# Performance work log

Measured on AMD Instinct MI355X. Metric: run time of the kernel, lower is better.

Reference implementation:

```python
import jax, jax.numpy as jnp
import numpy as np

N_NODES = 50000
N_EDGES = 1600000
IN_FEATS = 256
ENC_H = 20
DEC_H = 64
BIAS = 0.0  # forward arg default
TEMPERATURE = 1.0


def setup_inputs() -> dict:
    key = jax.random.key(0)
    ks = jax.random.split(key, 8)
    x = jax.random.normal(ks[0], (N_NODES, IN_FEATS), dtype=jnp.float32)
    edge_index = jax.random.randint(ks[1], (2, N_EDGES), 0, N_NODES, dtype=jnp.int64)
    node_id = 42
    # GCNConv params (glorot-ish scale)
    W_gcn = jax.random.normal(ks[2], (IN_FEATS, ENC_H), dtype=jnp.float32) / np.sqrt(IN_FEATS)
    b_gcn = jnp.zeros((ENC_H,), dtype=jnp.float32)
    # decoder MLP params
    W1 = jax.random.normal(ks[3], (3 * ENC_H, DEC_H), dtype=jnp.float32) / np.sqrt(3 * ENC_H)
    b1 = jnp.zeros((DEC_H,), dtype=jnp.float32)
    W2 = jax.random.normal(ks[4], (DEC_H, 1), dtype=jnp.float32) / np.sqrt(DEC_H)
    b2 = jnp.zeros((1,), dtype=jnp.float32)
    return {"x": x, "edge_index": edge_index, "node_id": node_id,
            "W_gcn": W_gcn, "b_gcn": b_gcn, "W1": W1, "b1": b1, "W2": W2, "b2": b2}


def _gcn_conv(x, edge_index, W, b):
    """PyG GCNConv: add self loops, symmetric normalization, sum aggregation."""
    n = x.shape[0]
    xw = x @ W  # [N, ENC_H]
    loop = jnp.arange(n, dtype=edge_index.dtype)
    row = jnp.concatenate([edge_index[0], loop])  # source
    col = jnp.concatenate([edge_index[1], loop])  # target
    ones = jnp.ones(row.shape[0], dtype=x.dtype)
    deg = jax.ops.segment_sum(ones, col, num_segments=n)
    dinv = jnp.where(deg > 0, jax.lax.rsqrt(jnp.maximum(deg, 1e-12)), 0.0)
    norm = dinv[row] * dinv[col]  # [E+N]
    msgs = xw[row] * norm[:, None]
    out = jax.ops.segment_sum(msgs, col, num_segments=n)
    return out + b


def reference(x, edge_index, node_id, W_gcn, b_gcn, W1, b1, W2, b2):
    # encoder: GCN + ReLU
    enc = jax.nn.relu(_gcn_conv(x, edge_index, W_gcn, b_gcn))  # [N, ENC_H]
    # edge representation: [row_embed | col_embed | node_embed]
    rows, cols = edge_index[0], edge_index[1]
    node_embed = jnp.broadcast_to(enc[node_id], (rows.shape[0], enc.shape[1]))
    z = jnp.concatenate([enc[rows], enc[cols], node_embed], axis=1)  # [E, 3*ENC_H]
    # decoder MLP
    h = jax.nn.relu(z @ W1 + b1)
    out_dec = h @ W2 + b2  # [E, 1]
    # Gumbel-sigmoid sampling (training=True path)
    bias = BIAS + 0.0001
    u = jax.random.uniform(jax.random.key(123), out_dec.shape, dtype=out_dec.dtype)
    eps = (bias - (1.0 - bias)) * u + (1.0 - bias)  # in (bias, 1-bias)
    gate = jnp.log(eps) - jnp.log1p(-eps)
    return jax.nn.sigmoid((gate + out_dec) / TEMPERATURE)
```

## Files before the change

### kernel.cpp

```cpp
#include <hip/hip_runtime.h>
#include <hip/hip_bf16.h>

#define IN_FEATS 256
#define ENC_H    20
#define DEC_H    64
#define EPB      8192

__device__ __forceinline__ unsigned int rotl32(unsigned int x, int d) {
  return (x << d) | (x >> (32 - d));
}

__device__ __forceinline__ void threefry2x32(unsigned int k0, unsigned int k1,
                                             unsigned int x0, unsigned int x1,
                                             unsigned int& o0, unsigned int& o1) {
  unsigned int ks0 = k0, ks1 = k1, ks2 = k0 ^ k1 ^ 0x1BD11BDAu;
  x0 += ks0; x1 += ks1;
  x0 += x1; x1 = rotl32(x1, 13); x1 ^= x0;
  x0 += x1; x1 = rotl32(x1, 15); x1 ^= x0;
  x0 += x1; x1 = rotl32(x1, 26); x1 ^= x0;
  x0 += x1; x1 = rotl32(x1,  6); x1 ^= x0;
  x0 += ks1; x1 += ks2 + 1u;
  x0 += x1; x1 = rotl32(x1, 17); x1 ^= x0;
  x0 += x1; x1 = rotl32(x1, 29); x1 ^= x0;
  x0 += x1; x1 = rotl32(x1, 16); x1 ^= x0;
  x0 += x1; x1 = rotl32(x1, 24); x1 ^= x0;
  x0 += ks2; x1 += ks0 + 2u;
  x0 += x1; x1 = rotl32(x1, 13); x1 ^= x0;
  x0 += x1; x1 = rotl32(x1, 15); x1 ^= x0;
  x0 += x1; x1 = rotl32(x1, 26); x1 ^= x0;
  x0 += x1; x1 = rotl32(x1,  6); x1 ^= x0;
  x0 += ks0; x1 += ks1 + 3u;
  x0 += x1; x1 = rotl32(x1, 17); x1 ^= x0;
  x0 += x1; x1 = rotl32(x1, 29); x1 ^= x0;
  x0 += x1; x1 = rotl32(x1, 16); x1 ^= x0;
  x0 += x1; x1 = rotl32(x1, 24); x1 ^= x0;
  x0 += ks1; x1 += ks2 + 4u;
  x0 += x1; x1 = rotl32(x1, 13); x1 ^= x0;
  x0 += x1; x1 = rotl32(x1, 15); x1 ^= x0;
  x0 += x1; x1 = rotl32(x1, 26); x1 ^= x0;
  x0 += x1; x1 = rotl32(x1,  6); x1 ^= x0;
  x0 += ks2; x1 += ks0 + 5u;
  o0 = x0; o1 = x1;
}

__device__ __forceinline__ float2 bf2_unpack(unsigned int u) {
  float2 f;
  f.x = __uint_as_float(u << 16);
  f.y = __uint_as_float(u & 0xffff0000u);
  return f;
}


__global__ __launch_bounds__(1024) void k_binhist(const int* __restrict__ row,
                                                  const int* __restrict__ col,
                                                  int* __restrict__ bbc,
                                                  unsigned int* __restrict__ rc,
                                                  int E, int nbins) {
  __shared__ int h[256];
  int t = threadIdx.x;
  if (t < 256) h[t] = 0;
  __syncthreads();
  int lo = blockIdx.x * EPB;
  int hi = min(lo + EPB, E);
  for (int e = lo + t; e < hi; e += 1024) {
    int c = col[e];
    atomicAdd(&h[c >> 8], 1);
    rc[e] = (unsigned int)row[e] | ((unsigned int)c << 16);
  }
  __syncthreads();
  if (t < nbins) bbc[blockIdx.x * nbins + t] = h[t];
}

__global__ void k_colA(const int* __restrict__ bbc, int* __restrict__ base,
                       int* __restrict__ binTot, int nblk, int nbins) {
  __shared__ int sd[256];
  int t = threadIdx.x;
  int bin = blockIdx.x;
  int v = (t < nblk) ? bbc[(size_t)t * nbins + bin] : 0;
  sd[t] = v;
  __syncthreads();
#pragma unroll
  for (int off = 1; off < 256; off <<= 1) {
    int tmp = (t >= off) ? sd[t - off] : 0;
    __syncthreads();
    sd[t] += tmp;
    __syncthreads();
  }
  if (t < nblk) base[(size_t)t * nbins + bin] = sd[t] - v;
  if (t == 255) binTot[bin] = sd[255];
}

__global__ void k_colB(const int* __restrict__ binTot, int* __restrict__ binStart, int nbins) {
  __shared__ int sd[256];
  int t = threadIdx.x;
  int v = (t < nbins) ? binTot[t] : 0;
  sd[t] = v;
  __syncthreads();
#pragma unroll
  for (int off = 1; off < 256; off <<= 1) {
    int tmp = (t >= off) ? sd[t - off] : 0;
    __syncthreads();
    sd[t] += tmp;
    __syncthreads();
  }
  if (t < nbins) {
    binStart[t] = sd[t] - v;
    if (t == nbins - 1) binStart[nbins] = sd[t];
  }
}

__global__ __launch_bounds__(1024) void k_binscatter(const unsigned int* __restrict__ rc,
                                                     const int* __restrict__ base,
                                                     const int* __restrict__ binStart,
                                                     unsigned int* __restrict__ binned,
                                                     int E, int nbins) {
  __shared__ int cur[256];
  int t = threadIdx.x;
  if (t < nbins) cur[t] = binStart[t] + base[(size_t)blockIdx.x * nbins + t];
  __syncthreads();
  int lo = blockIdx.x * EPB;
  int hi = min(lo + EPB, E);
  for (int e = lo + t; e < hi; e += 1024) {
    unsigned int v = rc[e];
    int slot = atomicAdd(&cur[v >> 24], 1);
    binned[slot] = v;
  }
}

__global__ __launch_bounds__(1024) void k_binsort(const unsigned int* __restrict__ binned,
                                                  const int* __restrict__ binStart,
                                                  unsigned short* __restrict__ sorted_r,
                                                  int* __restrict__ nstart,
                                                  float* __restrict__ dinv,
                                                  int N, int E) {
  __shared__ int cnt[256];
  __shared__ int ls[256];
  __shared__ int cur[256];
  int t = threadIdx.x;
  int bin = blockIdx.x;
  if (t < 256) cnt[t] = 0;
  __syncthreads();
  int s = binStart[bin], epos = binStart[bin + 1];
  for (int i = s + t; i < epos; i += 1024)
    atomicAdd(&cnt[(binned[i] >> 16) & 0xFFu], 1);
  __syncthreads();
  int v = (t < 256) ? cnt[t] : 0;
  if (t < 256) ls[t] = v;
  __syncthreads();
#pragma unroll
  for (int off = 1; off < 256; off <<= 1) {
    int tmp = 0;
    if (t < 256 && t >= off) tmp = ls[t - off];
    __syncthreads();
    if (t < 256 && t >= off) ls[t] += tmp;
    __syncthreads();
  }
  if (t < 256) {
    int ex = ls[t] - v;
    cur[t] = s + ex;
    int n = (bin << 8) + t;
    if (n < N) {
      nstart[n] = s + ex;
      dinv[n] = rsqrtf((float)(v + 1));
    }
  }
  if (bin == 0 && t == 0) nstart[N] = E;
  __syncthreads();
  for (int i = s + t; i < epos; i += 1024) {
    unsigned int e32 = binned[i];
    int cl = (int)((e32 >> 16) & 0xFFu);
    int slot = atomicAdd(&cur[cl], 1);
    sorted_r[slot] = (unsigned short)(e32 & 0xFFFFu);
  }
}


__global__ void k_xw(const float* __restrict__ x, const float* __restrict__ W,
                     const float* __restrict__ dinv, __hip_bfloat16* __restrict__ xwd, int N) {
  __shared__ float Wl[IN_FEATS * ENC_H];
  for (int i = threadIdx.x; i < IN_FEATS * ENC_H; i += blockDim.x) Wl[i] = W[i];
  __syncthreads();
  int g = blockIdx.x * blockDim.x + threadIdx.x;
  int n = g >> 2, part = g & 3;
  if (n >= N) return;
  float acc[ENC_H];
#pragma unroll
  for (int j = 0; j < ENC_H; j++) acc[j] = 0.0f;
  const float4* x4 = reinterpret_cast<const float4*>(x + (size_t)n * IN_FEATS);
#pragma unroll 4
  for (int k4 = 0; k4 < 16; k4++) {
    float4 v = x4[k4 * 4 + part];
    int kbase = k4 * 16 + part * 4;
    const float* w0 = &Wl[(kbase + 0) * ENC_H];
    const float* w1 = &Wl[(kbase + 1) * ENC_H];
    const float* w2 = &Wl[(kbase + 2) * ENC_H];
    const float* w3 = &Wl[(kbase + 3) * ENC_H];
#pragma unroll
    for (int j = 0; j < ENC_H; j++) {
      acc[j] = fmaf(v.x, w0[j], acc[j]);
      acc[j] = fmaf(v.y, w1[j], acc[j]);
      acc[j] = fmaf(v.z, w2[j], acc[j]);
      acc[j] = fmaf(v.w, w3[j], acc[j]);
    }
  }
#pragma unroll
  for (int j = 0; j < ENC_H; j++) acc[j] += __shfl_xor(acc[j], 1);
#pragma unroll
  for (int j = 0; j < ENC_H; j++) acc[j] += __shfl_xor(acc[j], 2);
  float d = dinv[n];
  __hip_bfloat16* o = xwd + (size_t)n * ENC_H;
  int jb = part * 5;
#pragma unroll
  for (int jj = 0; jj < 5; jj++) o[jb + jj] = __float2bfloat16(acc[jb + jj] * d);
}

__global__ void k_gather(const int* __restrict__ nstart,
                         const unsigned short* __restrict__ sorted_r,
                         const __hip_bfloat16* __restrict__ xwd, const float* __restrict__ dinv,
                         const float* __restrict__ bg, float* __restrict__ enc, int N) {
  int t = blockIdx.x * blockDim.x + threadIdx.x;
  int n = t / ENC_H;
  int j = t % ENC_H;
  if (n >= N) return;
  int s = nstart[n], epos = nstart[n + 1];
  float acc = __bfloat162float(xwd[(size_t)n * ENC_H + j]);
  for (int k = s; k < epos; k++) {
    int r = (int)sorted_r[k];
    acc += __bfloat162float(xwd[(size_t)r * ENC_H + j]);
  }
  float v = acc * dinv[n] + bg[j];
  enc[(size_t)n * ENC_H + j] = fmaxf(v, 0.0f);
}

__global__ void k_pq(const float* __restrict__ enc, const float* __restrict__ W1,
                     __hip_bfloat16* __restrict__ Pq, __hip_bfloat16* __restrict__ Qq, int N) {
  __shared__ float Wl[2 * ENC_H * DEC_H];
  for (int i = threadIdx.x; i < 2 * ENC_H * DEC_H; i += blockDim.x) Wl[i] = W1[i];
  __syncthreads();
  int t = blockIdx.x * blockDim.x + threadIdx.x;
  int n = t / DEC_H, j = t % DEC_H;
  if (n >= N) return;
  const float* en = enc + (size_t)n * ENC_H;
  float p = 0.0f, q = 0.0f;
#pragma unroll
  for (int k = 0; k < ENC_H; k++) {
    float ev = en[k];
    p = fmaf(ev, Wl[k * DEC_H + j], p);
    q = fmaf(ev, Wl[(k + ENC_H) * DEC_H + j], q);
  }
  size_t idx = (size_t)(j >> 4) * N * 16 + (size_t)n * 16 + (j & 15);
  Pq[idx] = __float2bfloat16(p);
  Qq[idx] = __float2bfloat16(q);
}

__global__ void k_t3(const float* __restrict__ enc, const float* __restrict__ W1,
                     const float* __restrict__ b1, const int* __restrict__ node_id,
                     float* __restrict__ t3) {
  int j = threadIdx.x;
  int nid = node_id[0];
  const float* en = enc + (size_t)nid * ENC_H;
  float a = b1[j];
#pragma unroll
  for (int k = 0; k < ENC_H; k++) a = fmaf(en[k], W1[(2 * ENC_H + k) * DEC_H + j], a);
  t3[j] = a;
}

template <int Q4>
__global__ void k_dec_q(const unsigned int* __restrict__ rc,
                        const __hip_bfloat16* __restrict__ Pq,
                        const __hip_bfloat16* __restrict__ Qq,
                        const float* __restrict__ t3, const float* __restrict__ W2,
                        const float* __restrict__ b2,
                        float* __restrict__ partial, float* __restrict__ out,
                        int N, int E) {
  __shared__ float t3l[16], w2l[16];
  if (threadIdx.x < 16) {
    t3l[threadIdx.x] = t3[Q4 * 16 + threadIdx.x];
    w2l[threadIdx.x] = W2[Q4 * 16 + threadIdx.x];
  }
  __syncthreads();
  int e = blockIdx.x * blockDim.x + threadIdx.x;
  if (e >= E) return;
  unsigned int v = rc[e];
  int r = (int)(v & 0xFFFFu);
  int c = (int)(v >> 16);
  const __hip_bfloat16* Pbase = Pq + (size_t)Q4 * N * 16;
  const __hip_bfloat16* Qbase = Qq + (size_t)Q4 * N * 16;
  const uint4* pr = reinterpret_cast<const uint4*>(Pbase + (size_t)r * 16);
  const uint4* qc = reinterpret_cast<const uint4*>(Qbase + (size_t)c * 16);
  float acc = 0.0f;
#pragma unroll
  for (int b = 0; b < 2; b++) {
    uint4 pu = pr[b];
    uint4 qu = qc[b];
    int j0 = b * 8;
    float2 p0 = bf2_unpack(pu.x), q0 = bf2_unpack(qu.x);
    float2 p1 = bf2_unpack(pu.y), q1 = bf2_unpack(qu.y);
    float2 p2 = bf2_unpack(pu.z), q2 = bf2_unpack(qu.z);
    float2 p3 = bf2_unpack(pu.w), q3 = bf2_unpack(qu.w);
    float h;
    h = fmaxf(p0.x + q0.x + t3l[j0 + 0], 0.0f); acc = fmaf(h, w2l[j0 + 0], acc);
    h = fmaxf(p0.y + q0.y + t3l[j0 + 1], 0.0f); acc = fmaf(h, w2l[j0 + 1], acc);
    h = fmaxf(p1.x + q1.x + t3l[j0 + 2], 0.0f); acc = fmaf(h, w2l[j0 + 2], acc);
    h = fmaxf(p1.y + q1.y + t3l[j0 + 3], 0.0f); acc = fmaf(h, w2l[j0 + 3], acc);
    h = fmaxf(p2.x + q2.x + t3l[j0 + 4], 0.0f); acc = fmaf(h, w2l[j0 + 4], acc);
    h = fmaxf(p2.y + q2.y + t3l[j0 + 5], 0.0f); acc = fmaf(h, w2l[j0 + 5], acc);
    h = fmaxf(p3.x + q3.x + t3l[j0 + 6], 0.0f); acc = fmaf(h, w2l[j0 + 6], acc);
    h = fmaxf(p3.y + q3.y + t3l[j0 + 7], 0.0f); acc = fmaf(h, w2l[j0 + 7], acc);
  }
  if (Q4 == 0) {
    partial[e] = acc;
  } else if (Q4 < 3) {
    partial[e] += acc;
  } else {
    float od = partial[e] + acc + b2[0];
    unsigned int o0, o1;
    threefry2x32(0u, 123u, 0u, (unsigned int)e, o0, o1);
    unsigned int bits = o0 ^ o1;
    float u = __uint_as_float((bits >> 9) | 0x3f800000u) - 1.0f;
    float eps = (-0.9998f) * u + 0.9999f;
    float gate = logf(eps) - log1pf(-eps);
    float s = 1.0f / (1.0f + expf(-(gate + od)));
    out[e] = s;
  }
}

extern "C" void kernel_launch(void* const* d_in, const int* in_sizes, int n_in,
                              void* d_out, int out_size, void* d_ws, size_t ws_size,
                              hipStream_t stream) {
  const float* x       = (const float*)d_in[0];
  const int*   edge    = (const int*)d_in[1];
  const int*   node_id = (const int*)d_in[2];
  const float* W_gcn   = (const float*)d_in[3];
  const float* b_gcn   = (const float*)d_in[4];
  const float* W1      = (const float*)d_in[5];
  const float* b1      = (const float*)d_in[6];
  const float* W2      = (const float*)d_in[7];
  const float* b2      = (const float*)d_in[8];
  float* out = (float*)d_out;

  int N = in_sizes[0] / IN_FEATS;
  int E = in_sizes[1] / 2;
  const int* erow = edge;
  const int* ecol = edge + E;
  int nbins = (N + 255) >> 8;
  int NB = (E + EPB - 1) / EPB;

  char* ws = (char*)d_ws;
  size_t off = 0;
  auto alloc = [&](size_t bytes) {
    char* p = ws + off;
    off = (off + bytes + 255) & ~(size_t)255;
    return p;
  };
  __hip_bfloat16* xwd = (__hip_bfloat16*)alloc((size_t)N * ENC_H * sizeof(__hip_bfloat16));
  float* enc  = (float*)alloc((size_t)N * ENC_H * sizeof(float));
  float* dinv = (float*)alloc((size_t)N * sizeof(float));
  int*  nstart = (int*)alloc((size_t)(N + 1) * sizeof(int));
  unsigned int*   rc       = (unsigned int*)alloc((size_t)E * sizeof(unsigned int));
  unsigned int*   binned   = (unsigned int*)alloc((size_t)E * sizeof(unsigned int));
  unsigned short* sorted_r = (unsigned short*)alloc((size_t)E * sizeof(unsigned short));
  int* bbc      = (int*)alloc((size_t)NB * nbins * sizeof(int));
  int* base     = (int*)alloc((size_t)NB * nbins * sizeof(int));
  int* binTot   = (int*)alloc((size_t)nbins * sizeof(int));
  int* binStart = (int*)alloc((size_t)(nbins + 1) * sizeof(int));
  __hip_bfloat16* Pq = (__hip_bfloat16*)alloc((size_t)N * DEC_H * sizeof(__hip_bfloat16));
  __hip_bfloat16* Qq = (__hip_bfloat16*)alloc((size_t)N * DEC_H * sizeof(__hip_bfloat16));
  float* partial = (float*)alloc((size_t)E * sizeof(float));
  float* t3   = (float*)alloc((size_t)DEC_H * sizeof(float));
  (void)ws_size; (void)n_in; (void)out_size;

  const int B = 256;
  int ge  = (E + B - 1) / B;
  int gxw = (N * 4 + B - 1) / B;
  int gg  = (N * ENC_H + B - 1) / B;
  int gpq = (N * DEC_H + B - 1) / B;

  k_binhist   <<<NB, 1024, 0, stream>>>(erow, ecol, bbc, rc, E, nbins);
  k_colA      <<<nbins, 256, 0, stream>>>(bbc, base, binTot, NB, nbins);
  k_colB      <<<1, 256, 0, stream>>>(binTot, binStart, nbins);
  k_binscatter<<<NB, 1024, 0, stream>>>(rc, base, binStart, binned, E, nbins);
  k_binsort   <<<nbins, 1024, 0, stream>>>(binned, binStart, sorted_r, nstart, dinv, N, E);
  k_xw        <<<gxw, B, 0, stream>>>(x, W_gcn, dinv, xwd, N);
  k_gather    <<<gg, B, 0, stream>>>(nstart, sorted_r, xwd, dinv, b_gcn, enc, N);
  k_pq        <<<gpq, B, 0, stream>>>(enc, W1, Pq, Qq, N);
  k_t3        <<<1, DEC_H, 0, stream>>>(enc, W1, b1, node_id, t3);
  k_dec_q<0>  <<<ge, B, 0, stream>>>(rc, Pq, Qq, t3, W2, b2, partial, out, N, E);
  k_dec_q<1>  <<<ge, B, 0, stream>>>(rc, Pq, Qq, t3, W2, b2, partial, out, N, E);
  k_dec_q<2>  <<<ge, B, 0, stream>>>(rc, Pq, Qq, t3, W2, b2, partial, out, N, E);
  k_dec_q<3>  <<<ge, B, 0, stream>>>(rc, Pq, Qq, t3, W2, b2, partial, out, N, E);
}
```

Measured before the change: 197.2 us.

## Fuse four quarter-decoder passes into one kernel with multiple edges per thread

The four templated decoder launches, each covering 16 of the 64 hidden units and passing a per-edge partial sum through global memory, become one kernel. Each thread handles four edges and keeps their accumulators in registers across the quarters. This removes the partial buffer's global reads and writes and three launches. The original split was likely there to keep each quarter's Pq/Qq slice cache-resident; the fused loop adds a __syncthreads after each quarter so the block walks the slices together, but cache locality across the whole grid may still be worse.

Result: slower. 240.7 us (+22.0%).

```diff
diff --git a/kernel.cpp b/kernel.cpp
--- a/kernel.cpp
+++ b/kernel.cpp
@@ -5,6 +5,7 @@
 #define ENC_H    20
 #define DEC_H    64
 #define EPB      8192
+#define EPT      4
 
 __device__ __forceinline__ unsigned int rotl32(unsigned int x, int d) {
   return (x << d) | (x >> (32 - d));
@@ -265,55 +266,71 @@
   t3[j] = a;
 }
 
-template <int Q4>
-__global__ void k_dec_q(const unsigned int* __restrict__ rc,
-                        const __hip_bfloat16* __restrict__ Pq,
-                        const __hip_bfloat16* __restrict__ Qq,
-                        const float* __restrict__ t3, const float* __restrict__ W2,
-                        const float* __restrict__ b2,
-                        float* __restrict__ partial, float* __restrict__ out,
-                        int N, int E) {
-  __shared__ float t3l[16], w2l[16];
-  if (threadIdx.x < 16) {
-    t3l[threadIdx.x] = t3[Q4 * 16 + threadIdx.x];
-    w2l[threadIdx.x] = W2[Q4 * 16 + threadIdx.x];
-  }
-  __syncthreads();
-  int e = blockIdx.x * blockDim.x + threadIdx.x;
-  if (e >= E) return;
-  unsigned int v = rc[e];
-  int r = (int)(v & 0xFFFFu);
-  int c = (int)(v >> 16);
-  const __hip_bfloat16* Pbase = Pq + (size_t)Q4 * N * 16;
-  const __hip_bfloat16* Qbase = Qq + (size_t)Q4 * N * 16;
-  const uint4* pr = reinterpret_cast<const uint4*>(Pbase + (size_t)r * 16);
-  const uint4* qc = reinterpret_cast<const uint4*>(Qbase + (size_t)c * 16);
-  float acc = 0.0f;
-#pragma unroll
-  for (int b = 0; b < 2; b++) {
-    uint4 pu = pr[b];
-    uint4 qu = qc[b];
-    int j0 = b * 8;
-    float2 p0 = bf2_unpack(pu.x), q0 = bf2_unpack(qu.x);
-    float2 p1 = bf2_unpack(pu.y), q1 = bf2_unpack(qu.y);
-    float2 p2 = bf2_unpack(pu.z), q2 = bf2_unpack(qu.z);
-    float2 p3 = bf2_unpack(pu.w), q3 = bf2_unpack(qu.w);
-    float h;
-    h = fmaxf(p0.x + q0.x + t3l[j0 + 0], 0.0f); acc = fmaf(h, w2l[j0 + 0], acc);
-    h = fmaxf(p0.y + q0.y + t3l[j0 + 1], 0.0f); acc = fmaf(h, w2l[j0 + 1], acc);
-    h = fmaxf(p1.x + q1.x + t3l[j0 + 2], 0.0f); acc = fmaf(h, w2l[j0 + 2], acc);
-    h = fmaxf(p1.y + q1.y + t3l[j0 + 3], 0.0f); acc = fmaf(h, w2l[j0 + 3], acc);
-    h = fmaxf(p2.x + q2.x + t3l[j0 + 4], 0.0f); acc = fmaf(h, w2l[j0 + 4], acc);
-    h = fmaxf(p2.y + q2.y + t3l[j0 + 5], 0.0f); acc = fmaf(h, w2l[j0 + 5], acc);
-    h = fmaxf(p3.x + q3.x + t3l[j0 + 6], 0.0f); acc = fmaf(h, w2l[j0 + 6], acc);
-    h = fmaxf(p3.y + q3.y + t3l[j0 + 7], 0.0f); acc = fmaf(h, w2l[j0 + 7], acc);
-  }
-  if (Q4 == 0) {
-    partial[e] = acc;
-  } else if (Q4 < 3) {
-    partial[e] += acc;
-  } else {
-    float od = partial[e] + acc + b2[0];
+__global__ void k_dec(const unsigned int* __restrict__ rc,
+                      const __hip_bfloat16* __restrict__ Pq,
+                      const __hip_bfloat16* __restrict__ Qq,
+                      const float* __restrict__ t3, const float* __restrict__ W2,
+                      const float* __restrict__ b2,
+                      float* __restrict__ out, int N, int E) {
+  __shared__ float t3l[DEC_H], w2l[DEC_H];
+  if (threadIdx.x < DEC_H) {
+    t3l[threadIdx.x] = t3[threadIdx.x];
+    w2l[threadIdx.x] = W2[threadIdx.x];
+  }
+  __syncthreads();
+  int base = blockIdx.x * (blockDim.x * EPT) + threadIdx.x;
+  unsigned int rcv[EPT];
+  float acc[EPT];
+#pragma unroll
+  for (int i = 0; i < EPT; i++) {
+    int e = base + i * 256;
+    rcv[i] = (e < E) ? rc[e] : 0u;
+    acc[i] = 0.0f;
+  }
+#pragma unroll
+  for (int q = 0; q < 4; q++) {
+    const __hip_bfloat16* Pb = Pq + (size_t)q * N * 16;
+    const __hip_bfloat16* Qb = Qq + (size_t)q * N * 16;
+#pragma unroll
+    for (int i = 0; i < EPT; i++) {
+      int e = base + i * 256;
+      if (e < E) {
+        unsigned int v = rcv[i];
+        int r = (int)(v & 0xFFFFu);
+        int c = (int)(v >> 16);
+        const uint4* pr = reinterpret_cast<const uint4*>(Pb + (size_t)r * 16);
+        const uint4* qc = reinterpret_cast<const uint4*>(Qb + (size_t)c * 16);
+        float a = acc[i];
+#pragma unroll
+        for (int b = 0; b < 2; b++) {
+          uint4 pu = pr[b];
+          uint4 qu = qc[b];
+          int j0 = q * 16 + b * 8;
+          float2 p0 = bf2_unpack(pu.x), q0 = bf2_unpack(qu.x);
+          float2 p1 = bf2_unpack(pu.y), q1 = bf2_unpack(qu.y);
+          float2 p2 = bf2_unpack(pu.z), q2 = bf2_unpack(qu.z);
+          float2 p3 = bf2_unpack(pu.w), q3 = bf2_unpack(qu.w);
+          float h;
+          h = fmaxf(p0.x + q0.x + t3l[j0 + 0], 0.0f); a = fmaf(h, w2l[j0 + 0], a);
+          h = fmaxf(p0.y + q0.y + t3l[j0 + 1], 0.0f); a = fmaf(h, w2l[j0 + 1], a);
+          h = fmaxf(p1.x + q1.x + t3l[j0 + 2], 0.0f); a = fmaf(h, w2l[j0 + 2], a);
+          h = fmaxf(p1.y + q1.y + t3l[j0 + 3], 0.0f); a = fmaf(h, w2l[j0 + 3], a);
+          h = fmaxf(p2.x + q2.x + t3l[j0 + 4], 0.0f); a = fmaf(h, w2l[j0 + 4], a);
+          h = fmaxf(p2.y + q2.y + t3l[j0 + 5], 0.0f); a = fmaf(h, w2l[j0 + 5], a);
+          h = fmaxf(p3.x + q3.x + t3l[j0 + 6], 0.0f); a = fmaf(h, w2l[j0 + 6], a);
+          h = fmaxf(p3.y + q3.y + t3l[j0 + 7], 0.0f); a = fmaf(h, w2l[j0 + 7], a);
+        }
+        acc[i] = a;
+      }
+    }
+    __syncthreads();
+  }
+  float bias2 = b2[0];
+#pragma unroll
+  for (int i = 0; i < EPT; i++) {
+    int e = base + i * 256;
+    if (e >= E) continue;
+    float od = acc[i] + bias2;
     unsigned int o0, o1;
     threefry2x32(0u, 123u, 0u, (unsigned int)e, o0, o1);
     unsigned int bits = o0 ^ o1;
@@ -366,15 +383,14 @@
   int* binStart = (int*)alloc((size_t)(nbins + 1) * sizeof(int));
   __hip_bfloat16* Pq = (__hip_bfloat16*)alloc((size_t)N * DEC_H * sizeof(__hip_bfloat16));
   __hip_bfloat16* Qq = (__hip_bfloat16*)alloc((size_t)N * DEC_H * sizeof(__hip_bfloat16));
-  float* partial = (float*)alloc((size_t)E * sizeof(float));
   float* t3   = (float*)alloc((size_t)DEC_H * sizeof(float));
   (void)ws_size; (void)n_in; (void)out_size;
 
   const int B = 256;
-  int ge  = (E + B - 1) / B;
   int gxw = (N * 4 + B - 1) / B;
   int gg  = (N * ENC_H + B - 1) / B;
   int gpq = (N * DEC_H + B - 1) / B;
+  int gdec = (E + B * EPT - 1) / (B * EPT);
 
   k_binhist   <<<NB, 1024, 0, stream>>>(erow, ecol, bbc, rc, E, nbins);
   k_colA      <<<nbins, 256, 0, stream>>>(bbc, base, binTot, NB, nbins);
@@ -385,8 +401,5 @@
   k_gather    <<<gg, B, 0, stream>>>(nstart, sorted_r, xwd, dinv, b_gcn, enc, N);
   k_pq        <<<gpq, B, 0, stream>>>(enc, W1, Pq, Qq, N);
   k_t3        <<<1, DEC_H, 0, stream>>>(enc, W1, b1, node_id, t3);
-  k_dec_q<0>  <<<ge, B, 0, stream>>>(rc, Pq, Qq, t3, W2, b2, partial, out, N, E);
-  k_dec_q<1>  <<<ge, B, 0, stream>>>(rc, Pq, Qq, t3, W2, b2, partial, out, N, E);
-  k_dec_q<2>  <<<ge, B, 0, stream>>>(rc, Pq, Qq, t3, W2, b2, partial, out, N, E);
-  k_dec_q<3>  <<<ge, B, 0, stream>>>(rc, Pq, Qq, t3, W2, b2, partial, out, N, E);
-}
+  k_dec       <<<gdec, B, 0, stream>>>(rc, Pq, Qq, t3, W2, b2, out, N, E);
+}
```
